# Optimization experiments

Measured on AMD Instinct MI355X. Metric: run time of the kernel, lower is better.

## Reference

```python
import jax, jax.numpy as jnp
import numpy as np

T, B, H, R = 4096, 32, 512, 512

def setup_inputs() -> dict:
    key = jax.random.key(0)
    k1, k2, k3, k4 = jax.random.split(key, 4)
    return {
        "encoded_contribution": jax.random.normal(k1, (T, B, H), dtype=jnp.float32),
        "mask": jnp.zeros((T, B), dtype=jnp.float32),
        "rnn_state": jax.random.normal(k2, (B, R), dtype=jnp.float32),
        "prev_att_weights": jnp.zeros((T, B), dtype=jnp.float32),
        "W_rec": jax.random.normal(k3, (H, R), dtype=jnp.float32) * 0.05,
        "w_score": jax.random.normal(k4, (H,), dtype=jnp.float32) * 0.05,
        "b_score": jnp.zeros((1,), dtype=jnp.float32),
    }

def reference(encoded_contribution, mask, rnn_state, prev_att_weights, W_rec, w_score, b_score):
    # rec_state_to_hidden (no bias): (B,R) @ (R,H) -> (B,H), broadcast over T
    rec = jnp.einsum('br,hr->bh', rnn_state, W_rec)
    hidden = encoded_contribution + rec[None, :, :]          # (T,B,H)
    # hidden_to_score: H -> 1, squeeze
    scores = jnp.einsum('tbh,h->tb', jnp.tanh(hidden), w_score) + b_score[0]
    scores = scores + mask                                    # additive mask (-1e5 for pad)
    att_weights = jax.nn.softmax(scores, axis=0)              # softmax over time T
    return att_weights
```

## Files before the change

kernel.cpp:

```cpp
#include <hip/hip_runtime.h>
#include <math.h>

typedef float vf4 __attribute__((ext_vector_type(4)));

__device__ __forceinline__ float wave_reduce_sum(float v) {
    #pragma unroll
    for (int off = 32; off > 0; off >>= 1)
        v += __shfl_xor(v, off, 64);
    return v;
}
__device__ __forceinline__ float wave_reduce_max(float v) {
    #pragma unroll
    for (int off = 32; off > 0; off >>= 1)
        v = fmaxf(v, __shfl_xor(v, off, 64));
    return v;
}

__device__ __forceinline__ float fast_tanh(float x) {
    float e = __expf(2.0f * x);
    return 1.0f - 2.0f * __builtin_amdgcn_rcpf(e + 1.0f);
}

__global__ void rec_kernel(const float* __restrict__ rnn,
                           const float* __restrict__ Wrec,
                           float* __restrict__ rec,
                           int B, int H, int R) {
    int w    = (blockIdx.x * blockDim.x + threadIdx.x) >> 6;
    int lane = threadIdx.x & 63;
    int nOut = B * H;
    if (w >= nOut) return;
    int b = w / H;
    int h = w - b * H;
    const float* xr = rnn  + (size_t)b * R;
    const float* wr = Wrec + (size_t)h * R;
    float acc = 0.f;
    for (int r = lane * 4; r < R; r += 256) {
        vf4 a = *(const vf4*)(xr + r);
        vf4 c = *(const vf4*)(wr + r);
        acc += a.x * c.x + a.y * c.y + a.z * c.z + a.w * c.w;
    }
    acc = wave_reduce_sum(acc);
    if (lane == 0) rec[w] = acc;
}

#define SCORE_ROWS 16
__global__ void score_kernel(const float* __restrict__ enc,
                             const float* __restrict__ mask,
                             const float* __restrict__ rec,
                             const float* __restrict__ wsc,
                             const float* __restrict__ bsc,
                             float* __restrict__ scores_t,
                             int T, int B, int H) {
    const int w    = (blockIdx.x * blockDim.x + threadIdx.x) >> 6;
    const int lane = threadIdx.x & 63;
    const int b     = w % B;
    const int tbase = (w / B) * SCORE_ROWS;
    if (tbase >= T) return;

    const int h0 = lane * 4;
    const int h1 = (H >> 1) + h0;

    const float* rr = rec + (size_t)b * H;
    vf4 r0 = *(const vf4*)(rr + h0);
    vf4 r1 = *(const vf4*)(rr + h1);
    vf4 w0 = *(const vf4*)(wsc + h0);
    vf4 w1 = *(const vf4*)(wsc + h1);
    const float bias = bsc[0];

    const float* erow = enc + ((size_t)tbase * B + b) * H;
    const size_t rstride = (size_t)B * H;

    float acc[SCORE_ROWS];
    #pragma unroll
    for (int i = 0; i < SCORE_ROWS; ++i) {
        const float* er = erow + (size_t)i * rstride;
        vf4 e0 = *(const vf4*)(er + h0);
        vf4 e1 = *(const vf4*)(er + h1);
        float a;
        a  = w0.x * fast_tanh(e0.x + r0.x);
        a += w0.y * fast_tanh(e0.y + r0.y);
        a += w0.z * fast_tanh(e0.z + r0.z);
        a += w0.w * fast_tanh(e0.w + r0.w);
        a += w1.x * fast_tanh(e1.x + r1.x);
        a += w1.y * fast_tanh(e1.y + r1.y);
        a += w1.z * fast_tanh(e1.z + r1.z);
        a += w1.w * fast_tanh(e1.w + r1.w);
        acc[i] = a;
    }

    #pragma unroll
    for (int s = 0; s < 4; ++s) {
        const int bit = 1 << s;
        #pragma unroll
        for (int i = 0; i < (SCORE_ROWS >> (s + 1)); ++i) {
            float sent = (lane & bit) ? acc[2 * i]     : acc[2 * i + 1];
            float keep = (lane & bit) ? acc[2 * i + 1] : acc[2 * i];
            acc[i] = keep + __shfl_xor(sent, bit, 64);
        }
    }
    acc[0] += __shfl_xor(acc[0], 16, 64);
    acc[0] += __shfl_xor(acc[0], 32, 64);

    if (lane < SCORE_ROWS) {
        const int t = tbase + lane;
        scores_t[(size_t)b * T + t] = acc[0] + bias + mask[(size_t)t * B + b];
    }
}

__global__ void stats_kernel(const float* __restrict__ scores_t,
                             float* __restrict__ stats, int T) {
    const int b    = blockIdx.x;
    const int tid  = threadIdx.x;
    const int wid  = tid >> 6;
    const int lane = tid & 63;
    const float* base = scores_t + (size_t)b * T;

    float m = -INFINITY;
    for (int i = tid * 4; i < T; i += 1024) {
        vf4 v = *(const vf4*)(base + i);
        m = fmaxf(m, fmaxf(fmaxf(v.x, v.y), fmaxf(v.z, v.w)));
    }
    m = wave_reduce_max(m);
    __shared__ float redm[4];
    if (lane == 0) redm[wid] = m;
    __syncthreads();
    m = fmaxf(fmaxf(redm[0], redm[1]), fmaxf(redm[2], redm[3]));

    float s = 0.f;
    for (int i = tid * 4; i < T; i += 1024) {
        vf4 v = *(const vf4*)(base + i);
        s += __expf(v.x - m) + __expf(v.y - m) + __expf(v.z - m) + __expf(v.w - m);
    }
    s = wave_reduce_sum(s);
    __shared__ float reds[4];
    if (lane == 0) reds[wid] = s;
    __syncthreads();
    if (tid == 0) {
        float ss = (reds[0] + reds[1]) + (reds[2] + reds[3]);
        stats[2 * b]     = m;
        stats[2 * b + 1] = 1.0f / ss;
    }
}

__global__ void finalize_kernel(const float* __restrict__ scores_t,
                                const float* __restrict__ stats,
                                float* __restrict__ out, int T, int B) {
    __shared__ float tile[32][65];
    __shared__ float sm[32];
    __shared__ float si[32];
    const int tid = threadIdx.x;
    const int t0  = blockIdx.x * 64;

    if (tid < B) {
        sm[tid] = stats[2 * tid];
        si[tid] = stats[2 * tid + 1];
    }
    __syncthreads();

    #pragma unroll
    for (int i = 0; i < 8; ++i) {
        int idx  = i * 256 + tid;
        int brow = idx >> 6;
        int tcol = idx & 63;
        tile[brow][tcol] = scores_t[(size_t)brow * T + t0 + tcol];
    }
    __syncthreads();

    #pragma unroll
    for (int i = 0; i < 8; ++i) {
        int idx  = i * 256 + tid;
        int trow = idx >> 5;
        int bcol = idx & 31;
        float x = tile[bcol][trow];
        float r = __expf(x - sm[bcol]) * si[bcol];
        out[(size_t)(t0 + trow) * B + bcol] = r;
    }
}

extern "C" void kernel_launch(void* const* d_in, const int* in_sizes, int n_in,
                              void* d_out, int out_size, void* d_ws, size_t ws_size,
                              hipStream_t stream) {
    const float* enc  = (const float*)d_in[0];
    const float* mask = (const float*)d_in[1];
    const float* rnn  = (const float*)d_in[2];
    const float* Wrec = (const float*)d_in[4];
    const float* wsc  = (const float*)d_in[5];
    const float* bsc  = (const float*)d_in[6];

    const int H = in_sizes[5];
    const int R = in_sizes[4] / H;
    const int B = in_sizes[2] / R;
    const int T = in_sizes[1] / B;

    float* rec      = (float*)d_ws;
    float* scores_t = rec + (size_t)B * H;
    float* stats    = scores_t + (size_t)B * T;
    float* out      = (float*)d_out;

    {
        int nOut   = B * H;
        int blocks = (nOut + 3) / 4;
        rec_kernel<<<blocks, 256, 0, stream>>>(rnn, Wrec, rec, B, H, R);
    }
    {
        int nWaves = (T / SCORE_ROWS) * B;
        int blocks = (nWaves + 3) / 4;
        score_kernel<<<blocks, 256, 0, stream>>>(enc, mask, rec, wsc, bsc,
                                                 scores_t, T, B, H);
    }
    stats_kernel<<<B, 1024, 0, stream>>>(scores_t, stats, T);
    finalize_kernel<<<T / 64, 256, 0, stream>>>(scores_t, stats, out, T, B);
}
```

Measured before the change: 56.06 us.

## Split softmax stats into per-chunk partials and widen score rows to 32

The softmax statistics pass now runs as B*8 blocks of 256 threads, each computing a local max and sum over a 512-element chunk, instead of 32 blocks of 1024 threads. The finalize kernel merges the partials with a rescaled log-sum-exp combine. This is meant to raise parallelism in the small stats stage. The score kernel also processes 32 time rows per wave, with one more shuffle-transpose reduction stage and launch bounds of 2, to amortize the rec and w loads, at the cost of more registers per thread.

Result: slower. 58.34 us (+4.1%).

```diff
diff --git a/kernel.cpp b/kernel.cpp
--- a/kernel.cpp
+++ b/kernel.cpp
@@ -1,7 +1,8 @@
 #include <hip/hip_runtime.h>
 #include <math.h>
 
-typedef float vf4 __attribute__((ext_vector_type(4)));
+typedef float  vf4 __attribute__((ext_vector_type(4)));
+typedef float  vf2 __attribute__((ext_vector_type(2)));
 
 __device__ __forceinline__ float wave_reduce_sum(float v) {
     #pragma unroll
@@ -43,14 +44,15 @@
     if (lane == 0) rec[w] = acc;
 }
 
-#define SCORE_ROWS 16
-__global__ void score_kernel(const float* __restrict__ enc,
-                             const float* __restrict__ mask,
-                             const float* __restrict__ rec,
-                             const float* __restrict__ wsc,
-                             const float* __restrict__ bsc,
-                             float* __restrict__ scores_t,
-                             int T, int B, int H) {
+#define SCORE_ROWS 32
+__global__ void __launch_bounds__(256, 2)
+score_kernel(const float* __restrict__ enc,
+             const float* __restrict__ mask,
+             const float* __restrict__ rec,
+             const float* __restrict__ wsc,
+             const float* __restrict__ bsc,
+             float* __restrict__ scores_t,
+             int T, int B, int H) {
     const int w    = (blockIdx.x * blockDim.x + threadIdx.x) >> 6;
     const int lane = threadIdx.x & 63;
     const int b     = w % B;
@@ -89,7 +91,7 @@
     }
 
     #pragma unroll
-    for (int s = 0; s < 4; ++s) {
+    for (int s = 0; s < 5; ++s) {
         const int bit = 1 << s;
         #pragma unroll
         for (int i = 0; i < (SCORE_ROWS >> (s + 1)); ++i) {
@@ -98,7 +100,6 @@
             acc[i] = keep + __shfl_xor(sent, bit, 64);
         }
     }
-    acc[0] += __shfl_xor(acc[0], 16, 64);
     acc[0] += __shfl_xor(acc[0], 32, 64);
 
     if (lane < SCORE_ROWS) {
@@ -107,43 +108,44 @@
     }
 }
 
-__global__ void stats_kernel(const float* __restrict__ scores_t,
-                             float* __restrict__ stats, int T) {
-    const int b    = blockIdx.x;
-    const int tid  = threadIdx.x;
+#define CHUNKS 8
+__global__ void stats_partial_kernel(const float* __restrict__ scores_t,
+                                     float* __restrict__ pm,
+                                     float* __restrict__ ps,
+                                     int T, int B) {
+    const int blk = blockIdx.x;
+    const int b   = blk % B;
+    const int c   = blk / B;
+    const int L   = T / CHUNKS;
+    const int tid = threadIdx.x;
     const int wid  = tid >> 6;
     const int lane = tid & 63;
-    const float* base = scores_t + (size_t)b * T;
-
-    float m = -INFINITY;
-    for (int i = tid * 4; i < T; i += 1024) {
-        vf4 v = *(const vf4*)(base + i);
-        m = fmaxf(m, fmaxf(fmaxf(v.x, v.y), fmaxf(v.z, v.w)));
-    }
+    const float* base = scores_t + (size_t)b * T + (size_t)c * L;
+
+    vf2 v = *(const vf2*)(base + tid * 2);
+
+    __shared__ float redm[4];
+    float m = fmaxf(v.x, v.y);
     m = wave_reduce_max(m);
-    __shared__ float redm[4];
     if (lane == 0) redm[wid] = m;
     __syncthreads();
     m = fmaxf(fmaxf(redm[0], redm[1]), fmaxf(redm[2], redm[3]));
 
-    float s = 0.f;
-    for (int i = tid * 4; i < T; i += 1024) {
-        vf4 v = *(const vf4*)(base + i);
-        s += __expf(v.x - m) + __expf(v.y - m) + __expf(v.z - m) + __expf(v.w - m);
-    }
+    float s = __expf(v.x - m) + __expf(v.y - m);
     s = wave_reduce_sum(s);
     __shared__ float reds[4];
     if (lane == 0) reds[wid] = s;
     __syncthreads();
     if (tid == 0) {
         float ss = (reds[0] + reds[1]) + (reds[2] + reds[3]);
-        stats[2 * b]     = m;
-        stats[2 * b + 1] = 1.0f / ss;
+        pm[c * B + b] = m;
+        ps[c * B + b] = ss;
     }
 }
 
 __global__ void finalize_kernel(const float* __restrict__ scores_t,
-                                const float* __restrict__ stats,
+                                const float* __restrict__ pm,
+                                const float* __restrict__ ps,
                                 float* __restrict__ out, int T, int B) {
     __shared__ float tile[32][65];
     __shared__ float sm[32];
@@ -152,8 +154,16 @@
     const int t0  = blockIdx.x * 64;
 
     if (tid < B) {
-        sm[tid] = stats[2 * tid];
-        si[tid] = stats[2 * tid + 1];
+        float m = -INFINITY;
+        #pragma unroll
+        for (int c = 0; c < CHUNKS; ++c)
+            m = fmaxf(m, pm[c * B + tid]);
+        float s = 0.f;
+        #pragma unroll
+        for (int c = 0; c < CHUNKS; ++c)
+            s += ps[c * B + tid] * __expf(pm[c * B + tid] - m);
+        sm[tid] = m;
+        si[tid] = 1.0f / s;
     }
     __syncthreads();
 
@@ -194,7 +204,8 @@
 
     float* rec      = (float*)d_ws;
     float* scores_t = rec + (size_t)B * H;
-    float* stats    = scores_t + (size_t)B * T;
+    float* pm       = scores_t + (size_t)B * T;
+    float* ps       = pm + (size_t)CHUNKS * B;
     float* out      = (float*)d_out;
 
     {
@@ -208,6 +219,6 @@
         score_kernel<<<blocks, 256, 0, stream>>>(enc, mask, rec, wsc, bsc,
                                                  scores_t, T, B, H);
     }
-    stats_kernel<<<B, 1024, 0, stream>>>(scores_t, stats, T);
-    finalize_kernel<<<T / 64, 256, 0, stream>>>(scores_t, stats, out, T, B);
-}
+    stats_partial_kernel<<<B * CHUNKS, 256, 0, stream>>>(scores_t, pm, ps, T, B);
+    finalize_kernel<<<T / 64, 256, 0, stream>>>(scores_t, pm, ps, out, T, B);
+}
```
